# Kernel tuning notes

Hardware: AMD Instinct MI355X
Metric: run time of the kernel (lower is better)

The kernel has to match this reference:

```python
import jax, jax.numpy as jnp
import numpy as np

N = 50000
E = 800000
IN_C = 128
HID = 8
OUT_C = 32
HEADS = (4, 4, 4)
NEG_SLOPE = 0.2


def gat_conv(x, src, dst, W, att_src, att_dst, bias, heads, out_c, concat):
    # x: [N, F_in]; W: [F_in, heads*out_c]; att_*: [heads, out_c]; bias: [heads*out_c] or [out_c]
    n = x.shape[0]
    h = (x @ W).reshape(n, heads, out_c)                      # [N, H, C]
    a_src = (h * att_src).sum(-1)                             # [N, H]
    a_dst = (h * att_dst).sum(-1)                             # [N, H]
    e = jax.nn.leaky_relu(a_src[src] + a_dst[dst], NEG_SLOPE)  # [E, H]
    # segment softmax over edges grouped by destination node
    m = jax.ops.segment_max(e, dst, num_segments=n)           # [N, H]
    m = jnp.where(jnp.isfinite(m), m, 0.0)
    p = jnp.exp(e - m[dst])                                   # [E, H]
    s = jax.ops.segment_sum(p, dst, num_segments=n)           # [N, H]
    alpha = p / (s[dst] + 1e-16)                              # [E, H]
    msg = h[src] * alpha[:, :, None]                          # [E, H, C]
    out = jax.ops.segment_sum(msg, dst, num_segments=n)       # [N, H, C]
    out = out.reshape(n, heads * out_c) if concat else out.mean(axis=1)
    return out + bias


def setup_inputs() -> dict:
    key = jax.random.key(0)
    ks = jax.random.split(key, 16)
    x = jax.random.normal(ks[0], (N, IN_C), dtype=jnp.float32)
    edge_index = jax.random.randint(ks[1], (2, E), 0, N, dtype=jnp.int64)
    c1 = HID                       # per-head out of conv1 (8)
    c2 = HID * HEADS[0]            # per-head out of conv2 (32)
    c3 = OUT_C                     # per-head out of conv3 (32)
    in2 = HID * HEADS[0]           # 32
    in3 = HID * HEADS[0] * HEADS[1]  # 128
    sc = 0.1
    return {
        "x": x,
        "edge_index": edge_index,
        "W1": jax.random.normal(ks[2], (IN_C, HEADS[0] * c1), dtype=jnp.float32) * sc,
        "as1": jax.random.normal(ks[3], (HEADS[0], c1), dtype=jnp.float32) * sc,
        "ad1": jax.random.normal(ks[4], (HEADS[0], c1), dtype=jnp.float32) * sc,
        "b1": jnp.zeros((HEADS[0] * c1,), dtype=jnp.float32),
        "W2": jax.random.normal(ks[5], (in2, HEADS[1] * c2), dtype=jnp.float32) * sc,
        "as2": jax.random.normal(ks[6], (HEADS[1], c2), dtype=jnp.float32) * sc,
        "ad2": jax.random.normal(ks[7], (HEADS[1], c2), dtype=jnp.float32) * sc,
        "b2": jnp.zeros((HEADS[1] * c2,), dtype=jnp.float32),
        "W3": jax.random.normal(ks[8], (in3, HEADS[2] * c3), dtype=jnp.float32) * sc,
        "as3": jax.random.normal(ks[9], (HEADS[2], c3), dtype=jnp.float32) * sc,
        "ad3": jax.random.normal(ks[10], (HEADS[2], c3), dtype=jnp.float32) * sc,
        "b3": jnp.zeros((c3,), dtype=jnp.float32),
    }


def reference(x, edge_index, W1, as1, ad1, b1, W2, as2, ad2, b2, W3, as3, ad3, b3):
    src, dst = edge_index[0], edge_index[1]
    h = gat_conv(x, src, dst, W1, as1, ad1, b1, HEADS[0], HID, True)
    h = jax.nn.elu(h)
    h = gat_conv(h, src, dst, W2, as2, ad2, b2, HEADS[1], HID * HEADS[0], True)
    h = jax.nn.elu(h)
    out = gat_conv(h, src, dst, W3, as3, ad3, b3, HEADS[2], OUT_C, False)
    return out
```

## Files before the change

kernel.cpp:

```cpp
#include <hip/hip_runtime.h>
#include <hip/hip_fp16.h>

#define NEG_SLOPE 0.2f

static inline int cdiv(long long a, long long b) { return (int)((a + b - 1) / b); }

typedef _Float16 f16x8 __attribute__((ext_vector_type(8)));
typedef float f32x4 __attribute__((ext_vector_type(4)));

union h8u {
    f16x8   v;
    __half2 h2[4];
};

__device__ __forceinline__ void load_sd(const void* ei_raw, int is64, int e, int E_,
                                        int& s, int& d)
{
    if (is64) {
        const long long* p = (const long long*)ei_raw;
        s = (int)p[e];
        d = (int)p[E_ + e];
    } else {
        const int* p = (const int*)ei_raw;
        s = p[e];
        d = p[E_ + e];
    }
}

__global__ __launch_bounds__(256) void prep_kernel(
    const void* __restrict__ ei, int E_, int n, int* __restrict__ flag,
    int* __restrict__ deg,
    const float* __restrict__ W1, __half* __restrict__ Wt1,
    const float* __restrict__ W2, __half* __restrict__ Wt2,
    const float* __restrict__ W3, __half* __restrict__ Wt3)
{
    int idx = blockIdx.x * 256 + threadIdx.x;

    if (blockIdx.x == 0) {
        __shared__ int bad;
        if (threadIdx.x == 0) bad = 0;
        __syncthreads();
        const long long* e64 = (const long long*)ei;
        int cnt = E_ < 512 ? E_ : 512;
        bool ok = true;
        for (int i = threadIdx.x; i < cnt; i += 256) {
            long long v = e64[i];
            if (v < 0 || v >= n) ok = false;
        }
        if (!ok) atomicAdd(&bad, 1);
        __syncthreads();
        if (threadIdx.x == 0) *flag = (bad == 0) ? 1 : 0;
    }

    if (idx < n) deg[idx] = 0;

    if (idx < 128 * 32) {
        int k = idx / 32, c = idx % 32;
        Wt1[c * 128 + k] = __float2half(W1[idx]);
    }
    if (idx < 32 * 128) {
        int k = idx / 128, c = idx % 128;
        Wt2[c * 32 + k] = __float2half(W2[idx]);
    }
    if (idx < 128 * 128) {
        int k = idx / 128, c = idx % 128;
        Wt3[c * 128 + k] = __float2half(W3[idx]);
    }
}

__global__ __launch_bounds__(256) void gemm1_hist_kernel(
    const float* __restrict__ x, const __half* __restrict__ Wt1,
    const float* __restrict__ att_s, const float* __restrict__ att_d,
    __half* __restrict__ h, float* __restrict__ a_s, float* __restrict__ a_d,
    int n, int gemmBlocks,
    const void* __restrict__ ei, const int* __restrict__ flag,
    int* __restrict__ deg, unsigned short* __restrict__ s16,
    unsigned short* __restrict__ d16, unsigned short* __restrict__ r16, int E_)
{
    constexpr int KC = 32, NT = 2, XP = 40, HP = 40, C = 8;
    __shared__ _Float16 Xs[64 * XP];
    __shared__ _Float16 Ws[32 * XP];
    __shared__ _Float16 Hs[64 * HP];
    __shared__ float As[32], Ad[32];

    const int tid = threadIdx.x;

    if (blockIdx.x >= gemmBlocks) {
        int base = (blockIdx.x - gemmBlocks) * 1024 + tid;
        int is64 = *flag;
        int sj[4], dj[4], rj[4];
        bool v[4];
#pragma unroll
        for (int j = 0; j < 4; j++) {
            int e = base + j * 256;
            v[j] = e < E_;
            if (v[j]) load_sd(ei, is64, e, E_, sj[j], dj[j]);
        }
#pragma unroll
        for (int j = 0; j < 4; j++) {
            int e = base + j * 256;
            if (v[j]) {
                s16[e] = (unsigned short)sj[j];
                d16[e] = (unsigned short)dj[j];
            }
        }
#pragma unroll
        for (int j = 0; j < 4; j++) {
            if (v[j]) rj[j] = atomicAdd(deg + dj[j], 1);
        }
#pragma unroll
        for (int j = 0; j < 4; j++) {
            int e = base + j * 256;
            if (v[j]) r16[e] = (unsigned short)rj[j];
        }
        return;
    }

    const int nb   = blockIdx.x * 64;
    const int wave = tid >> 6, lane = tid & 63;
    const int m16  = lane & 15, quad = lane >> 4;

    if (tid < 32) { As[tid] = att_s[tid]; Ad[tid] = att_d[tid]; }

    f32x4 acc[NT];
#pragma unroll
    for (int t = 0; t < NT; t++) acc[t] = (f32x4){0.f, 0.f, 0.f, 0.f};

    for (int kc = 0; kc < 128; kc += KC) {
        {
            int node = tid >> 2, seg = tid & 3;
            int gn = nb + node;
            f16x8 v = {0, 0, 0, 0, 0, 0, 0, 0};
            if (gn < n) {
                const float4* p = (const float4*)(x + (size_t)gn * 128 + kc + seg * 8);
                float4 a = p[0], b = p[1];
                v = (f16x8){(_Float16)a.x, (_Float16)a.y, (_Float16)a.z, (_Float16)a.w,
                            (_Float16)b.x, (_Float16)b.y, (_Float16)b.z, (_Float16)b.w};
            }
            *(f16x8*)&Xs[node * XP + seg * 8] = v;
        }
        if (tid < 32 * 4) {
            int col = tid >> 2, seg = tid & 3;
            *(f16x8*)&Ws[col * XP + seg * 8] =
                *(const f16x8*)(Wt1 + (size_t)col * 128 + kc + seg * 8);
        }
        __syncthreads();

        f16x8 a = *(const f16x8*)&Xs[(wave * 16 + m16) * XP + quad * 8];
#pragma unroll
        for (int t = 0; t < NT; t++) {
            f16x8 b = *(const f16x8*)&Ws[(t * 16 + m16) * XP + quad * 8];
            acc[t] = __builtin_amdgcn_mfma_f32_16x16x32_f16(a, b, acc[t], 0, 0, 0);
        }
        __syncthreads();
    }

#pragma unroll
    for (int t = 0; t < NT; t++) {
#pragma unroll
        for (int r = 0; r < 4; r++) {
            int row = wave * 16 + quad * 4 + r;
            Hs[row * HP + t * 16 + m16] = (_Float16)acc[t][r];
        }
    }
    __syncthreads();

    if (tid < 64 * 4) {
        int row = tid >> 2, seg = tid & 3;
        int gn = nb + row;
        if (gn < n)
            *(f16x8*)(h + (size_t)gn * 32 + seg * 8) =
                *(const f16x8*)&Hs[row * HP + seg * 8];
    }

    {
        int node = tid >> 2, head = tid & 3;
        int gn = nb + node;
        const _Float16* hr = &Hs[node * HP + head * C];
        float s1 = 0.f, s2 = 0.f;
#pragma unroll
        for (int c = 0; c < C; c++) {
            float v = (float)hr[c];
            s1 += v * As[head * C + c];
            s2 += v * Ad[head * C + c];
        }
        if (gn < n) {
            a_s[gn * 4 + head] = s1;
            a_d[gn * 4 + head] = s2;
        }
    }
}

__device__ __forceinline__ int wave_incl_scan(int v)
{
    int lane = threadIdx.x & 63;
#pragma unroll
    for (int off = 1; off < 64; off <<= 1) {
        int t = __shfl_up(v, off);
        if (lane >= off) v += t;
    }
    return v;
}

__global__ __launch_bounds__(1024) void scan_part_kernel(const int* __restrict__ deg,
                                                         int* __restrict__ start,
                                                         int* __restrict__ bsum, int n)
{
    __shared__ int wsum[16];
    int i = blockIdx.x * 1024 + threadIdx.x;
    int wid = threadIdx.x >> 6, lane = threadIdx.x & 63;
    int v = (i < n) ? deg[i] : 0;
    int incl = wave_incl_scan(v);
    if (lane == 63) wsum[wid] = incl;
    __syncthreads();
    if (wid == 0) {
        int w = (lane < 16) ? wsum[lane] : 0;
        w = wave_incl_scan(w);
        if (lane < 16) wsum[lane] = w;
    }
    __syncthreads();
    int excl = incl - v + (wid ? wsum[wid - 1] : 0);
    if (i < n) start[i] = excl;
    if (threadIdx.x == 1023) bsum[blockIdx.x] = wsum[15];
}

__global__ __launch_bounds__(1024) void scan_add_kernel(const int* __restrict__ deg,
                                                        const int* __restrict__ bsum,
                                                        int* __restrict__ start, int n)
{
    __shared__ int off_sh;
    if (threadIdx.x == 0) {
        int s = 0;
        for (int j = 0; j < blockIdx.x; j++) s += bsum[j];
        off_sh = s;
    }
    __syncthreads();
    int i = blockIdx.x * 1024 + threadIdx.x;
    if (i >= n) return;
    int v = start[i] + off_sh;
    start[i] = v;
    if (i == n - 1) start[n] = v + deg[i];
}

__global__ __launch_bounds__(256) void scatter_kernel(
    const unsigned short* __restrict__ s16, const unsigned short* __restrict__ d16,
    const unsigned short* __restrict__ r16, const int* __restrict__ start,
    unsigned short* __restrict__ sorted_src, int E_)
{
    int base = blockIdx.x * 1024 + threadIdx.x;
    int sj[4], dj[4], rj[4];
    bool v[4];
#pragma unroll
    for (int j = 0; j < 4; j++) {
        int e = base + j * 256;
        v[j] = e < E_;
        sj[j] = v[j] ? (int)s16[e] : 0;
        dj[j] = v[j] ? (int)d16[e] : 0;
        rj[j] = v[j] ? (int)r16[e] : 0;
    }
    int pj[4];
#pragma unroll
    for (int j = 0; j < 4; j++) {
        if (v[j]) pj[j] = start[dj[j]] + rj[j];
    }
#pragma unroll
    for (int j = 0; j < 4; j++) {
        if (v[j])
            __builtin_nontemporal_store((unsigned short)sj[j], sorted_src + pj[j]);
    }
}

template <int K, int NOUT>
__global__ __launch_bounds__(256) void gemm_mfma_kernel(
    const __half* __restrict__ xin, const __half* __restrict__ Wt,
    const float* __restrict__ att_s, const float* __restrict__ att_d,
    __half* __restrict__ h, float* __restrict__ a_s, float* __restrict__ a_d, int n)
{
    constexpr int KC = 32;
    constexpr int NT = NOUT / 16;
    constexpr int XP = KC + 8;
    constexpr int HP = NOUT + 8;
    constexpr int C  = NOUT / 4;

    __shared__ _Float16 Xs[64 * XP];
    __shared__ _Float16 Ws[NOUT * XP];
    __shared__ _Float16 Hs[64 * HP];
    __shared__ float As[NOUT], Ad[NOUT];

    const int tid  = threadIdx.x;
    const int nb   = blockIdx.x * 64;
    const int wave = tid >> 6, lane = tid & 63;
    const int m16  = lane & 15, quad = lane >> 4;

    if (tid < NOUT) { As[tid] = att_s[tid]; Ad[tid] = att_d[tid]; }

    f32x4 acc[NT];
#pragma unroll
    for (int t = 0; t < NT; t++) acc[t] = (f32x4){0.f, 0.f, 0.f, 0.f};

    for (int kc = 0; kc < K; kc += KC) {
        {
            int node = tid >> 2, seg = tid & 3;
            int gn = nb + node;
            f16x8 v = {0, 0, 0, 0, 0, 0, 0, 0};
            if (gn < n)
                v = *(const f16x8*)(xin + (size_t)gn * K + kc + seg * 8);
            *(f16x8*)&Xs[node * XP + seg * 8] = v;
        }
        for (int u = tid; u < NOUT * 4; u += 256) {
            int col = u >> 2, seg = u & 3;
            *(f16x8*)&Ws[col * XP + seg * 8] =
                *(const f16x8*)(Wt + (size_t)col * K + kc + seg * 8);
        }
        __syncthreads();

        f16x8 a = *(const f16x8*)&Xs[(wave * 16 + m16) * XP + quad * 8];
#pragma unroll
        for (int t = 0; t < NT; t++) {
            f16x8 b = *(const f16x8*)&Ws[(t * 16 + m16) * XP + quad * 8];
            acc[t] = __builtin_amdgcn_mfma_f32_16x16x32_f16(a, b, acc[t], 0, 0, 0);
        }
        __syncthreads();
    }

#pragma unroll
    for (int t = 0; t < NT; t++) {
#pragma unroll
        for (int r = 0; r < 4; r++) {
            int row = wave * 16 + quad * 4 + r;
            Hs[row * HP + t * 16 + m16] = (_Float16)acc[t][r];
        }
    }
    __syncthreads();

    for (int u = tid; u < 64 * NOUT / 8; u += 256) {
        int row = u / (NOUT / 8), seg = u % (NOUT / 8);
        int gn = nb + row;
        if (gn < n)
            *(f16x8*)(h + (size_t)gn * NOUT + seg * 8) =
                *(const f16x8*)&Hs[row * HP + seg * 8];
    }

    {
        int node = tid >> 2, head = tid & 3;
        int gn = nb + node;
        const _Float16* hr = &Hs[node * HP + head * C];
        float s1 = 0.f, s2 = 0.f;
#pragma unroll 4
        for (int c = 0; c < C; c++) {
            float v = (float)hr[c];
            s1 += v * As[head * C + c];
            s2 += v * Ad[head * C + c];
        }
        if (gn < n) {
            a_s[gn * 4 + head] = s1;
            a_d[gn * 4 + head] = s2;
        }
    }
}

template <int MODE>
__global__ __launch_bounds__(256) void gat_agg128_kernel(
    const int* __restrict__ start, const unsigned short* __restrict__ ss,
    const __half* __restrict__ h, const float* __restrict__ a_s,
    const float* __restrict__ a_d, const float* __restrict__ bias,
    void* __restrict__ out, int n)
{
    int local = threadIdx.x >> 4;
    int q     = threadIdx.x & 15;
    int node  = blockIdx.x * 16 + local;
    bool active = node < n;
    int s0 = 0, s1 = 0;
    if (active) { s0 = start[node]; s1 = start[node + 1]; }
    int head = q >> 2;
    float adh = active ? a_d[node * 4 + head] : 0.f;
    const f16x8* __restrict__ h8 = (const f16x8*)h + q;

    float acc[8];
#pragma unroll
    for (int j = 0; j < 8; j++) acc[j] = 0.f;
    float sm = 0.f;

    int i = s0;
    for (; i + 8 <= s1; i += 8) {
        int   sj[8];
        float ej[8];
        h8u   rj[8];
#pragma unroll
        for (int j = 0; j < 8; j++) sj[j] = (int)ss[i + j];
#pragma unroll
        for (int j = 0; j < 8; j++) ej[j] = a_s[sj[j] * 4 + head];
#pragma unroll
        for (int j = 0; j < 8; j++) rj[j].v = h8[(size_t)sj[j] * 16];
#pragma unroll
        for (int j = 0; j < 8; j++) {
            float e = ej[j] + adh;
            e = e > 0.f ? e : NEG_SLOPE * e;
            float p = __expf(e);
            sm += p;
#pragma unroll
            for (int k = 0; k < 4; k++) {
                float2 f = __half22float2(rj[j].h2[k]);
                acc[2 * k]     += f.x * p;
                acc[2 * k + 1] += f.y * p;
            }
        }
    }
    for (; i < s1; i++) {
        int s = (int)ss[i];
        float e = a_s[s * 4 + head] + adh;
        e = e > 0.f ? e : NEG_SLOPE * e;
        float p = __expf(e);
        sm += p;
        h8u u; u.v = h8[(size_t)s * 16];
#pragma unroll
        for (int k = 0; k < 4; k++) {
            float2 f = __half22float2(u.h2[k]);
            acc[2 * k]     += f.x * p;
            acc[2 * k + 1] += f.y * p;
        }
    }

    float inv = 1.f / (sm + 1e-16f);
#pragma unroll
    for (int j = 0; j < 8; j++) acc[j] *= inv;

    if (MODE == 0) {
        if (active) {
            h8u u;
#pragma unroll
            for (int k = 0; k < 4; k++) {
                float vx = acc[2 * k]     + bias[q * 8 + 2 * k];
                float vy = acc[2 * k + 1] + bias[q * 8 + 2 * k + 1];
                vx = vx > 0.f ? vx : (__expf(vx) - 1.f);
                vy = vy > 0.f ? vy : (__expf(vy) - 1.f);
                u.h2[k] = __floats2half2_rn(vx, vy);
            }
            *(f16x8*)((__half*)out + (size_t)node * 128 + q * 8) = u.v;
        }
    } else {
        __shared__ float sh[16][132];
#pragma unroll
        for (int j = 0; j < 8; j++) sh[local][q * 8 + j] = acc[j];
        __syncthreads();
        if (q < 4 && active) {
            float r[8];
#pragma unroll
            for (int j = 0; j < 8; j++) {
                int c = q * 8 + j;
                r[j] = 0.25f * (sh[local][c] + sh[local][32 + c] + sh[local][64 + c] +
                                sh[local][96 + c]) + bias[c];
            }
            float4* o4 = (float4*)((float*)out + (size_t)node * 32 + q * 8);
            o4[0] = make_float4(r[0], r[1], r[2], r[3]);
            o4[1] = make_float4(r[4], r[5], r[6], r[7]);
        }
    }
}

__global__ __launch_bounds__(256) void gat_agg32_kernel(
    const int* __restrict__ start, const unsigned short* __restrict__ ss,
    const __half* __restrict__ h, const float* __restrict__ a_s,
    const float* __restrict__ a_d, const float* __restrict__ bias,
    __half* __restrict__ out, int n)
{
    int local = threadIdx.x >> 2;
    int q     = threadIdx.x & 3;
    int node  = blockIdx.x * 64 + local;
    bool active = node < n;
    int s0 = 0, s1 = 0;
    if (active) { s0 = start[node]; s1 = start[node + 1]; }
    float adh = active ? a_d[node * 4 + q] : 0.f;
    const f16x8* __restrict__ h8 = (const f16x8*)h + q;

    float acc[8];
#pragma unroll
    for (int j = 0; j < 8; j++) acc[j] = 0.f;
    float sm = 0.f;

    int i = s0;
    for (; i + 8 <= s1; i += 8) {
        int   sj[8];
        float ej[8];
        h8u   rj[8];
#pragma unroll
        for (int j = 0; j < 8; j++) sj[j] = (int)ss[i + j];
#pragma unroll
        for (int j = 0; j < 8; j++) ej[j] = a_s[sj[j] * 4 + q];
#pragma unroll
        for (int j = 0; j < 8; j++) rj[j].v = h8[(size_t)sj[j] * 4];
#pragma unroll
        for (int j = 0; j < 8; j++) {
            float e = ej[j] + adh;
            e = e > 0.f ? e : NEG_SLOPE * e;
            float p = __expf(e);
            sm += p;
#pragma unroll
            for (int k = 0; k < 4; k++) {
                float2 f = __half22float2(rj[j].h2[k]);
                acc[2 * k]     += f.x * p;
                acc[2 * k + 1] += f.y * p;
            }
        }
    }
    for (; i < s1; i++) {
        int s = (int)ss[i];
        float e = a_s[s * 4 + q] + adh;
        e = e > 0.f ? e : NEG_SLOPE * e;
        float p = __expf(e);
        sm += p;
        h8u u; u.v = h8[(size_t)s * 4];
#pragma unroll
        for (int k = 0; k < 4; k++) {
            float2 f = __half22float2(u.h2[k]);
            acc[2 * k]     += f.x * p;
            acc[2 * k + 1] += f.y * p;
        }
    }

    if (active) {
        float inv = 1.f / (sm + 1e-16f);
        h8u u;
#pragma unroll
        for (int k = 0; k < 4; k++) {
            float vx = acc[2 * k] * inv     + bias[q * 8 + 2 * k];
            float vy = acc[2 * k + 1] * inv + bias[q * 8 + 2 * k + 1];
            vx = vx > 0.f ? vx : (__expf(vx) - 1.f);
            vy = vy > 0.f ? vy : (__expf(vy) - 1.f);
            u.h2[k] = __floats2half2_rn(vx, vy);
        }
        *(f16x8*)(out + (size_t)node * 32 + q * 8) = u.v;
    }
}


extern "C" void kernel_launch(void* const* d_in, const int* in_sizes, int n_in,
                              void* d_out, int out_size, void* d_ws, size_t ws_size,
                              hipStream_t stream)
{
    const float* x   = (const float*)d_in[0];
    const void*  ei  = d_in[1];
    const float* W1  = (const float*)d_in[2];
    const float* as1 = (const float*)d_in[3];
    const float* ad1 = (const float*)d_in[4];
    const float* b1  = (const float*)d_in[5];
    const float* W2  = (const float*)d_in[6];
    const float* as2 = (const float*)d_in[7];
    const float* ad2 = (const float*)d_in[8];
    const float* b2  = (const float*)d_in[9];
    const float* W3  = (const float*)d_in[10];
    const float* as3 = (const float*)d_in[11];
    const float* ad3 = (const float*)d_in[12];
    const float* b3  = (const float*)d_in[13];
    float* out = (float*)d_out;

    const int N_ = in_sizes[0] / 128;
    const int E_ = in_sizes[1] / 2;

    char* ws = (char*)d_ws;
    size_t off = 0;
    auto alloc = [&](size_t nbytes) -> void* {
        void* p = ws + off;
        off += (nbytes + 255) & ~(size_t)255;
        return p;
    };
    __half* h          = (__half*)alloc((size_t)N_ * 128 * 2);
    __half* x2h        = (__half*)alloc((size_t)N_ * 32 * 2);
    __half* x3h        = (__half*)alloc((size_t)N_ * 128 * 2);
    __half* Wt1        = (__half*)alloc(128 * 32 * 2);
    __half* Wt2        = (__half*)alloc(32 * 128 * 2);
    __half* Wt3        = (__half*)alloc(128 * 128 * 2);
    float* asrc        = (float*)alloc((size_t)N_ * 4 * 4);
    float* adst        = (float*)alloc((size_t)N_ * 4 * 4);
    int*   deg         = (int*)alloc((size_t)N_ * 4);
    int*   start       = (int*)alloc((size_t)(N_ + 1) * 4);
    unsigned short* sorted_src = (unsigned short*)alloc((size_t)E_ * 2);
    unsigned short* s16        = (unsigned short*)alloc((size_t)E_ * 2);
    unsigned short* d16        = (unsigned short*)alloc((size_t)E_ * 2);
    unsigned short* r16        = (unsigned short*)alloc((size_t)E_ * 2);
    int*   bsum        = (int*)alloc(4096);
    int*   flag        = (int*)alloc(256);

    const int gN16  = cdiv(N_, 16);
    const int gN64  = cdiv(N_, 64);
    const int gHist = cdiv(E_, 1024);
    const int nSB   = cdiv(N_, 1024);
    int prepWork = N_ > 128 * 128 ? N_ : 128 * 128;

    prep_kernel<<<cdiv(prepWork, 256), 256, 0, stream>>>(ei, E_, N_, flag, deg,
                                                         W1, Wt1, W2, Wt2, W3, Wt3);
    gemm1_hist_kernel<<<gN64 + gHist, 256, 0, stream>>>(
        x, Wt1, as1, ad1, h, asrc, adst, N_, gN64,
        ei, flag, deg, s16, d16, r16, E_);
    scan_part_kernel<<<nSB, 1024, 0, stream>>>(deg, start, bsum, N_);
    scan_add_kernel<<<nSB, 1024, 0, stream>>>(deg, bsum, start, N_);
    scatter_kernel<<<cdiv(E_, 1024), 256, 0, stream>>>(s16, d16, r16, start,
                                                       sorted_src, E_);

    gat_agg32_kernel<<<gN64, 256, 0, stream>>>(start, sorted_src, h, asrc, adst, b1,
                                               x2h, N_);

    gemm_mfma_kernel<32, 128><<<gN64, 256, 0, stream>>>(x2h, Wt2, as2, ad2, h,
                                                        asrc, adst, N_);
    gat_agg128_kernel<0><<<gN16, 256, 0, stream>>>(start, sorted_src, h, asrc, adst, b2,
                                                   x3h, N_);

    gemm_mfma_kernel<128, 128><<<gN64, 256, 0, stream>>>(x3h, Wt3, as3, ad3, h,
                                                         asrc, adst, N_);
    gat_agg128_kernel<1><<<gN16, 256, 0, stream>>>(start, sorted_src, h, asrc, adst, b3,
                                                   out, N_);
}
```

Measured before the change: 277.3 us.

## Privatize degree histogram into 8 copies to reduce atomic contention

Splits the per-destination degree counter into 8 partitioned copies chosen by block index, so edge-histogram atomics spread across more addresses. A new combine kernel computes per-partition offsets and total degrees, and the scatter kernel uses the packed partition id and rank to place edges. This adds an extra kernel launch, 8x larger zeroing and an extra gather in scatter. Ranks are limited to 12 bits, and sorted order within each node changes.

New measurement: 284.3 us. 1.03x slower.

```diff
diff --git a/kernel.cpp b/kernel.cpp
--- a/kernel.cpp
+++ b/kernel.cpp
@@ -29,7 +29,7 @@
 
 __global__ __launch_bounds__(256) void prep_kernel(
     const void* __restrict__ ei, int E_, int n, int* __restrict__ flag,
-    int* __restrict__ deg,
+    int* __restrict__ degP,
     const float* __restrict__ W1, __half* __restrict__ Wt1,
     const float* __restrict__ W2, __half* __restrict__ Wt2,
     const float* __restrict__ W3, __half* __restrict__ Wt3)
@@ -52,7 +52,7 @@
         if (threadIdx.x == 0) *flag = (bad == 0) ? 1 : 0;
     }
 
-    if (idx < n) deg[idx] = 0;
+    if (idx < 8 * n) degP[idx] = 0;
 
     if (idx < 128 * 32) {
         int k = idx / 32, c = idx % 32;
@@ -74,7 +74,7 @@
     __half* __restrict__ h, float* __restrict__ a_s, float* __restrict__ a_d,
     int n, int gemmBlocks,
     const void* __restrict__ ei, const int* __restrict__ flag,
-    int* __restrict__ deg, unsigned short* __restrict__ s16,
+    int* __restrict__ degP, unsigned short* __restrict__ s16,
     unsigned short* __restrict__ d16, unsigned short* __restrict__ r16, int E_)
 {
     constexpr int KC = 32, NT = 2, XP = 40, HP = 40, C = 8;
@@ -86,6 +86,8 @@
     const int tid = threadIdx.x;
 
     if (blockIdx.x >= gemmBlocks) {
+        int g = blockIdx.x & 7;
+        int* deg_g = degP + (size_t)g * n;
         int base = (blockIdx.x - gemmBlocks) * 1024 + tid;
         int is64 = *flag;
         int sj[4], dj[4], rj[4];
@@ -106,12 +108,12 @@
         }
 #pragma unroll
         for (int j = 0; j < 4; j++) {
-            if (v[j]) rj[j] = atomicAdd(deg + dj[j], 1);
+            if (v[j]) rj[j] = atomicAdd(deg_g + dj[j], 1);
         }
 #pragma unroll
         for (int j = 0; j < 4; j++) {
             int e = base + j * 256;
-            if (v[j]) r16[e] = (unsigned short)rj[j];
+            if (v[j]) r16[e] = (unsigned short)(rj[j] | (g << 12));
         }
         return;
     }
@@ -191,6 +193,21 @@
     }
 }
 
+__global__ __launch_bounds__(256) void combine_kernel(const int* __restrict__ degP,
+                                                      unsigned short* __restrict__ off8,
+                                                      int* __restrict__ deg, int n)
+{
+    int i = blockIdx.x * 256 + threadIdx.x;
+    if (i >= n) return;
+    int sum = 0;
+#pragma unroll
+    for (int g = 0; g < 8; g++) {
+        off8[(size_t)g * n + i] = (unsigned short)sum;
+        sum += degP[(size_t)g * n + i];
+    }
+    deg[i] = sum;
+}
+
 __device__ __forceinline__ int wave_incl_scan(int v)
 {
     int lane = threadIdx.x & 63;
@@ -245,10 +262,11 @@
 __global__ __launch_bounds__(256) void scatter_kernel(
     const unsigned short* __restrict__ s16, const unsigned short* __restrict__ d16,
     const unsigned short* __restrict__ r16, const int* __restrict__ start,
-    unsigned short* __restrict__ sorted_src, int E_)
+    const unsigned short* __restrict__ off8,
+    unsigned short* __restrict__ sorted_src, int n, int E_)
 {
     int base = blockIdx.x * 1024 + threadIdx.x;
-    int sj[4], dj[4], rj[4];
+    int sj[4], dj[4], rr[4];
     bool v[4];
 #pragma unroll
     for (int j = 0; j < 4; j++) {
@@ -256,12 +274,16 @@
         v[j] = e < E_;
         sj[j] = v[j] ? (int)s16[e] : 0;
         dj[j] = v[j] ? (int)d16[e] : 0;
-        rj[j] = v[j] ? (int)r16[e] : 0;
+        rr[j] = v[j] ? (int)r16[e] : 0;
     }
     int pj[4];
 #pragma unroll
     for (int j = 0; j < 4; j++) {
-        if (v[j]) pj[j] = start[dj[j]] + rj[j];
+        if (v[j]) {
+            int g = rr[j] >> 12;
+            int rank = rr[j] & 0xFFF;
+            pj[j] = start[dj[j]] + (int)off8[(size_t)g * n + dj[j]] + rank;
+        }
     }
 #pragma unroll
     for (int j = 0; j < 4; j++) {
@@ -572,8 +594,10 @@
     __half* Wt3        = (__half*)alloc(128 * 128 * 2);
     float* asrc        = (float*)alloc((size_t)N_ * 4 * 4);
     float* adst        = (float*)alloc((size_t)N_ * 4 * 4);
+    int*   degP        = (int*)alloc((size_t)8 * N_ * 4);
     int*   deg         = (int*)alloc((size_t)N_ * 4);
     int*   start       = (int*)alloc((size_t)(N_ + 1) * 4);
+    unsigned short* off8       = (unsigned short*)alloc((size_t)8 * N_ * 2);
     unsigned short* sorted_src = (unsigned short*)alloc((size_t)E_ * 2);
     unsigned short* s16        = (unsigned short*)alloc((size_t)E_ * 2);
     unsigned short* d16        = (unsigned short*)alloc((size_t)E_ * 2);
@@ -585,17 +609,18 @@
     const int gN64  = cdiv(N_, 64);
     const int gHist = cdiv(E_, 1024);
     const int nSB   = cdiv(N_, 1024);
-    int prepWork = N_ > 128 * 128 ? N_ : 128 * 128;
-
-    prep_kernel<<<cdiv(prepWork, 256), 256, 0, stream>>>(ei, E_, N_, flag, deg,
+    int prepWork = 8 * N_ > 128 * 128 ? 8 * N_ : 128 * 128;
+
+    prep_kernel<<<cdiv(prepWork, 256), 256, 0, stream>>>(ei, E_, N_, flag, degP,
                                                          W1, Wt1, W2, Wt2, W3, Wt3);
     gemm1_hist_kernel<<<gN64 + gHist, 256, 0, stream>>>(
         x, Wt1, as1, ad1, h, asrc, adst, N_, gN64,
-        ei, flag, deg, s16, d16, r16, E_);
+        ei, flag, degP, s16, d16, r16, E_);
+    combine_kernel<<<cdiv(N_, 256), 256, 0, stream>>>(degP, off8, deg, N_);
     scan_part_kernel<<<nSB, 1024, 0, stream>>>(deg, start, bsum, N_);
     scan_add_kernel<<<nSB, 1024, 0, stream>>>(deg, bsum, start, N_);
-    scatter_kernel<<<cdiv(E_, 1024), 256, 0, stream>>>(s16, d16, r16, start,
-                                                       sorted_src, E_);
+    scatter_kernel<<<cdiv(E_, 1024), 256, 0, stream>>>(s16, d16, r16, start, off8,
+                                                       sorted_src, N_, E_);
 
     gat_agg32_kernel<<<gN64, 256, 0, stream>>>(start, sorted_src, h, asrc, adst, b1,
                                                x2h, N_);
```
